# Kernel tuning notes

Measured on AMD Instinct MI355X. Metric: run time of the kernel, lower is better.

Reference implementation:

```python
import jax, jax.numpy as jnp
import numpy as np

NUM_EMB = 1024
DIM = 256
BETA = 0.25


def setup_inputs() -> dict:
    key = jax.random.key(0)
    kx, kc = jax.random.split(key)
    x = jax.random.normal(kx, (32, DIM, 32, 32), dtype=jnp.float32)
    # nn.Parameter(...).uniform_(-1/num_emb, 1/num_emb)
    code_book = jax.random.uniform(kc, (NUM_EMB, DIM), dtype=jnp.float32,
                                   minval=-1.0 / NUM_EMB, maxval=1.0 / NUM_EMB)
    return {"x": x, "code_book": code_book}


def reference(x, code_book):
    b, c, h, w = x.shape
    # (b h w) c
    x_ = x.transpose(0, 2, 3, 1).reshape(-1, c)
    sq = jnp.sum(code_book ** 2, axis=-1)[None, :] + jnp.sum(x_ ** 2, axis=-1)[:, None]
    dist = sq - 2.0 * jnp.einsum('nc,kc->nk', x_, code_book)
    ids = jnp.argmin(dist, axis=-1).reshape(b, h, w)
    emb = code_book[ids]            # [b, h, w, c]
    emb = emb.transpose(0, 3, 1, 2)  # [b, c, h, w]
    dict_loss = jnp.mean((jax.lax.stop_gradient(x) - emb) ** 2)
    commitment_loss = BETA * jnp.mean((x - jax.lax.stop_gradient(emb)) ** 2)
    emb_loss = dict_loss + commitment_loss
    # straight-through estimator
    emb_st = x + jax.lax.stop_gradient(emb - x)
    return ids, emb_st, emb_loss
```

## Files before the change

kernel.cpp:

```cpp
#include <hip/hip_runtime.h>

#define NUM_EMB 1024
#define DIM     256
#define NPIX    32768
#define NELEM   8388608

typedef unsigned short u16;
typedef unsigned int   u32;
typedef __attribute__((ext_vector_type(8))) _Float16 f16x8;
typedef __attribute__((ext_vector_type(4))) float f32x4;

__device__ __forceinline__ u16 f32_f16(float f) {
    _Float16 h = (_Float16)f;
    return __builtin_bit_cast(u16, h);
}
__device__ __forceinline__ float f16_f32(u16 b) {
    return (float)__builtin_bit_cast(_Float16, b);
}


__global__ __launch_bounds__(256) void k_prep_x(const float* __restrict__ x,
        u16* __restrict__ Xa, u16* __restrict__ Xb,
        float* __restrict__ nx_out)
{
    __shared__ float nxp[4][64];
    const int t  = threadIdx.x;
    const int p  = t & 63;
    const int cq = t >> 6;
    const int bi = blockIdx.x;
    const int b  = bi >> 4;
    const int hw = ((bi & 15) << 6) + p;
    const float* xp = x + (((size_t)(b * 256 + cq * 64)) << 10) + hw;
    float s = 0.f;
    for (int i0 = 0; i0 < 64; i0 += 8) {
        u32 qa[4], qb[4];
#pragma unroll
        for (int j = 0; j < 8; ++j) {
            float v = xp[(size_t)(i0 + j) << 10];
            s = fmaf(v, v, s);
            float va = v * 0.25f;
            u16 ha = f32_f16(va);
            float rb = (va - f16_f32(ha)) * 1024.0f;
            u16 hb = f32_f16(rb);
            if ((j & 1) == 0) { qa[j>>1] = ha; qb[j>>1] = hb; }
            else { qa[j>>1] |= (u32)ha << 16; qb[j>>1] |= (u32)hb << 16; }
        }
        const int c = cq * 64 + i0;
        const size_t chunk = (((size_t)((c >> 5) * 4 + ((c >> 3) & 3))) << 15)
                             + (size_t)bi * 64 + p;
        *(uint4*)(Xa + chunk * 8) = make_uint4(qa[0], qa[1], qa[2], qa[3]);
        *(uint4*)(Xb + chunk * 8) = make_uint4(qb[0], qb[1], qb[2], qb[3]);
    }
    nxp[cq][p] = s;
    __syncthreads();
    if (t < 64)
        nx_out[bi * 64 + t] = ((nxp[0][t] + nxp[1][t]) + nxp[2][t]) + nxp[3][t];
}

__global__ __launch_bounds__(256) void k_prep_e(const float* __restrict__ cb,
        u16* __restrict__ Ea, u16* __restrict__ Eb,
        float* __restrict__ ne_out)
{
    const int t = threadIdx.x;
    const int l32 = t & 31;
    const int code = blockIdx.x * 8 + (t >> 5);
    const float* cp = cb + (size_t)code * 256 + l32 * 8;
    u32 qa[4], qb[4];
    float s = 0.f;
#pragma unroll
    for (int j = 0; j < 8; ++j) {
        float v = cp[j];
        s = fmaf(v, v, s);
        float va = v * 2048.0f;
        u16 ha = f32_f16(va);
        float rb = (va - f16_f32(ha)) * 1024.0f;
        u16 hb = f32_f16(rb);
        if ((j & 1) == 0) { qa[j>>1] = ha; qb[j>>1] = hb; }
        else { qa[j>>1] |= (u32)ha << 16; qb[j>>1] |= (u32)hb << 16; }
    }
    const size_t chunk = ((size_t)l32 << 10) + code;
    *(uint4*)(Ea + chunk * 8) = make_uint4(qa[0], qa[1], qa[2], qa[3]);
    *(uint4*)(Eb + chunk * 8) = make_uint4(qb[0], qb[1], qb[2], qb[3]);
#pragma unroll
    for (int off = 16; off > 0; off >>= 1) s += __shfl_xor(s, off);
    if (l32 == 0) ne_out[code] = s;
}

__global__ __launch_bounds__(256, 4) void k_mfma_argmin(
        const u16* __restrict__ XA, const u16* __restrict__ XB,
        const u16* __restrict__ EA, const u16* __restrict__ EB,
        const float* __restrict__ nx, const float* __restrict__ ne,
        float* __restrict__ partV, int* __restrict__ partI)
{
    __shared__ __align__(16) unsigned char ldsA[2][8192];
    __shared__ float redV[4][64];
    __shared__ int   redI[4][64];

    const int t = threadIdx.x;
    const int l = t & 63;
    const int w = t >> 6;

    const int bi   = blockIdx.x;
    const int xcd  = bi & 7;
    const int slot = bi >> 3;
    const int cT   = slot & 7;
    const int pT   = ((slot >> 3) << 3) | xcd;
    const int px0  = pT << 6;
    const int c0   = cT << 7;
    const int n0   = w << 5;
    const int kbl  = l >> 4;
    const int il   = l & 15;

    const u16* Xt[2] = {XA, XB};

    auto stageA = [&](int kc, int bf) {
#pragma unroll
        for (int q = 0; q < 2; ++q) {
            const int kb = t >> 6, px = t & 63;
            const u16* sa = Xt[q] + ((((size_t)(kc * 4 + kb)) << 15) + px0 + px) * 8;
            __builtin_amdgcn_global_load_lds(
                (const __attribute__((address_space(1))) void*)sa,
                (__attribute__((address_space(3))) void*)(&ldsA[bf][q * 4096 + t * 16]),
                16, 0, 0);
        }
    };

    f32x4 acc1[4][2], acc2[4][2];
#pragma unroll
    for (int i = 0; i < 4; ++i)
#pragma unroll
        for (int j = 0; j < 2; ++j) {
            acc1[i][j] = (f32x4){0.f, 0.f, 0.f, 0.f};
            acc2[i][j] = (f32x4){0.f, 0.f, 0.f, 0.f};
        }

    const size_t boff = (size_t)kbl * 8192 + (size_t)(c0 + n0 + il) * 8;
    const u16* pBa = EA + boff;
    const u16* pBb = EB + boff;

    f16x8 bqa[2], bqb[2];
#pragma unroll
    for (int ni = 0; ni < 2; ++ni) {
        bqa[ni] = *(const f16x8*)(pBa + ni * 128);
        bqb[ni] = *(const f16x8*)(pBb + ni * 128);
    }
    stageA(0, 0);
    __syncthreads();

#pragma unroll
    for (int kc = 0; kc < 8; ++kc) {
        const int bf = kc & 1;
        if (kc < 7) stageA(kc + 1, bf ^ 1);

        f16x8 nqa[2], nqb[2];
        if (kc < 7) {
#pragma unroll
            for (int ni = 0; ni < 2; ++ni) {
                nqa[ni] = *(const f16x8*)(pBa + (size_t)(kc + 1) * 32768 + ni * 128);
                nqb[ni] = *(const f16x8*)(pBb + (size_t)(kc + 1) * 32768 + ni * 128);
            }
        }

        __builtin_amdgcn_s_setprio(1);
#pragma unroll
        for (int mi = 0; mi < 4; ++mi) {
            const int fo = (kbl * 64 + mi * 16 + il) * 16;
            f16x8 afa = *(const f16x8*)(&ldsA[bf][fo]);
            f16x8 afb = *(const f16x8*)(&ldsA[bf][4096 + fo]);
#pragma unroll
            for (int ni = 0; ni < 2; ++ni) {
                acc1[mi][ni] = __builtin_amdgcn_mfma_f32_16x16x32_f16(
                    afa, bqa[ni], acc1[mi][ni], 0, 0, 0);
                acc2[mi][ni] = __builtin_amdgcn_mfma_f32_16x16x32_f16(
                    afb, bqa[ni], acc2[mi][ni], 0, 0, 0);
                acc2[mi][ni] = __builtin_amdgcn_mfma_f32_16x16x32_f16(
                    afa, bqb[ni], acc2[mi][ni], 0, 0, 0);
            }
        }
        __builtin_amdgcn_s_setprio(0);

        if (kc < 7) {
            __syncthreads();
#pragma unroll
            for (int ni = 0; ni < 2; ++ni) { bqa[ni] = nqa[ni]; bqb[ni] = nqb[ni]; }
        }
    }

    const int g = kbl, col = il;
    float nev[2];
#pragma unroll
    for (int ni = 0; ni < 2; ++ni) nev[ni] = ne[c0 + n0 + ni * 16 + col];
#pragma unroll
    for (int mi = 0; mi < 4; ++mi) {
#pragma unroll
        for (int r = 0; r < 4; ++r) {
            const int pxl = mi * 16 + g * 4 + r;
            const float nxv = nx[px0 + pxl];
            float best = 3.4e38f; int besti = 0;
#pragma unroll
            for (int ni = 0; ni < 2; ++ni) {
                float tt = fmaf(acc2[mi][ni][r], 9.765625e-04f, acc1[mi][ni][r]);
                float sc = (nxv + nev[ni]) - tt * 3.90625e-03f;
                if (sc < best) { best = sc; besti = c0 + n0 + ni * 16 + col; }
            }
#pragma unroll
            for (int off = 1; off < 16; off <<= 1) {
                float ov = __shfl_xor(best, off);
                int   oi = __shfl_xor(besti, off);
                if (ov < best || (ov == best && oi < besti)) { best = ov; besti = oi; }
            }
            if (col == 0) { redV[w][pxl] = best; redI[w][pxl] = besti; }
        }
    }
    __syncthreads();
    if (t < 64) {
        float bv = redV[0][t]; int bidx = redI[0][t];
#pragma unroll
        for (int q = 1; q < 4; ++q) {
            float v = redV[q][t];
            int   i = redI[q][t];
            if (v < bv || (v == bv && i < bidx)) { bv = v; bidx = i; }
        }
        partV[cT * NPIX + px0 + t] = bv;
        partI[cT * NPIX + px0 + t] = bidx;
    }
}

__global__ __launch_bounds__(256) void k_outputs2(const float* __restrict__ x,
        const float* __restrict__ cb,
        const float* __restrict__ partV, const int* __restrict__ partI,
        float* __restrict__ ids_f, float* __restrict__ out_emb,
        float* __restrict__ partials)
{
    __shared__ int   ids_s[64];
    __shared__ float ev[64][65];
    __shared__ float sm[256];

    const int t  = threadIdx.x;
    const int w  = t >> 6, l = t & 63;
    const int bi = blockIdx.x;
    const int b  = bi >> 4;
    const int hw0 = (bi & 15) << 6;
    const int n0 = (b << 10) + hw0;

    if (t < 64) {
        const int px = n0 + t;
        float bv = partV[px]; int bix = partI[px];
#pragma unroll
        for (int ct = 1; ct < 8; ++ct) {
            float v = partV[ct * NPIX + px];
            int   i = partI[ct * NPIX + px];
            if (v < bv || (v == bv && i < bix)) { bv = v; bix = i; }
        }
        ids_f[px] = (float)bix;
        ids_s[t] = bix;
    }
    __syncthreads();

    float s = 0.f;
    for (int cc = 0; cc < 4; ++cc) {
#pragma unroll
        for (int pp = 0; pp < 16; ++pp) {
            const int px = w * 16 + pp;
            ev[px][l] = cb[(size_t)ids_s[px] * DIM + cc * 64 + l];
        }
        __syncthreads();
#pragma unroll
        for (int ci = 0; ci < 16; ++ci) {
            const int c  = cc * 64 + w * 16 + ci;
            const size_t xi = (((size_t)(b * DIM + c)) << 10) + hw0 + l;
            float xv = x[xi];
            float e  = ev[l][c & 63];
            out_emb[xi] = xv + (e - xv);
            float d = xv - e;
            s = fmaf(d, d, s);
        }
        __syncthreads();
    }
    sm[t] = s;
    __syncthreads();
    for (int off = 128; off > 0; off >>= 1) {
        if (t < off) sm[t] += sm[t + off];
        __syncthreads();
    }
    if (t == 0) partials[bi] = sm[0];
}

__global__ __launch_bounds__(256) void k_finalize(const float* __restrict__ partials,
                                                  int nparts,
                                                  float* __restrict__ out_loss)
{
    __shared__ float sm[256];
    const int tid = threadIdx.x;
    float s = 0.f;
    for (int k = tid; k < nparts; k += 256) s += partials[k];
    sm[tid] = s;
    __syncthreads();
    for (int off = 128; off > 0; off >>= 1) {
        if (tid < off) sm[tid] += sm[tid + off];
        __syncthreads();
    }
    if (tid == 0) {
        float m = sm[0] / (float)NELEM;
        out_loss[0] = m + 0.25f * m;
    }
}

__global__ __launch_bounds__(256) void k_enorm(const float* __restrict__ cb,
                                               float* __restrict__ enorm)
{
    const int tid  = threadIdx.x;
    const int lane = tid & 63;
    const int w    = tid >> 6;
    const int k    = blockIdx.x * 4 + w;
    const float* cp = cb + (size_t)k * DIM;
    float s = 0.f;
#pragma unroll
    for (int t = 0; t < 4; ++t) {
        float v = cp[lane + t * 64];
        s = fmaf(v, v, s);
    }
#pragma unroll
    for (int off = 32; off > 0; off >>= 1) s += __shfl_down(s, off);
    if (lane == 0) enorm[k] = s;
}

__global__ __launch_bounds__(256) void k_argmin(const float* __restrict__ x,
                                                const float* __restrict__ cb,
                                                const float* __restrict__ enorm,
                                                float* __restrict__ out_ids)
{
    __shared__ float xs[32][64];
    __shared__ float cbs[32][68];
    __shared__ float nx_l[64];
    __shared__ float nxp[4][64];
    __shared__ float red_v[64][17];
    __shared__ int   red_i[64][17];

    const int tid  = threadIdx.x;
    const int tx   = tid & 15;
    const int ty   = tid >> 4;
    const int pix0 = blockIdx.x * 64;
    const int b    = pix0 >> 10;
    const int hw0  = pix0 & 1023;

    {
        const int p = tid & 63, q = tid >> 6;
        float s = 0.f;
        const float* xp = x + ((size_t)(b * DIM + q * 64) * 1024) + hw0 + p;
        for (int c = 0; c < 64; ++c) {
            float v = xp[c * 1024];
            s = fmaf(v, v, s);
        }
        nxp[q][p] = s;
        __syncthreads();
        if (tid < 64)
            nx_l[tid] = ((nxp[0][tid] + nxp[1][tid]) + nxp[2][tid]) + nxp[3][tid];
        __syncthreads();
    }

    float nx_r[4];
#pragma unroll
    for (int i = 0; i < 4; ++i) nx_r[i] = nx_l[ty * 4 + i];

    float best_v[4];
    int   best_i[4];
#pragma unroll
    for (int i = 0; i < 4; ++i) { best_v[i] = 3.4e38f; best_i[i] = 0; }

    for (int cc = 0; cc < 16; ++cc) {
        float acc[4][4];
#pragma unroll
        for (int i = 0; i < 4; ++i)
#pragma unroll
            for (int j = 0; j < 4; ++j) acc[i][j] = 0.f;

        for (int kcc = 0; kcc < 8; ++kcc) {
            __syncthreads();
            {
                const int p = tid & 63, k0 = tid >> 6;
                const float* xp = x + ((size_t)(b * DIM + kcc * 32) * 1024) + hw0 + p;
#pragma unroll
                for (int tt = 0; tt < 8; ++tt) {
                    int kk = k0 + tt * 4;
                    xs[kk][p] = xp[kk * 1024];
                }
            }
            {
                const int kk = tid & 31, r0 = tid >> 5;
                const float* cp = cb + (size_t)(cc * 64) * DIM + kcc * 32 + kk;
#pragma unroll
                for (int tt = 0; tt < 8; ++tt) {
                    int r = r0 + tt * 8;
                    cbs[kk][r] = cp[r * DIM];
                }
            }
            __syncthreads();
#pragma unroll
            for (int kk = 0; kk < 32; ++kk) {
                float4 A = *(const float4*)&xs[kk][ty * 4];
                float4 B = *(const float4*)&cbs[kk][tx * 4];
                float a[4] = {A.x, A.y, A.z, A.w};
                float bb[4] = {B.x, B.y, B.z, B.w};
#pragma unroll
                for (int i = 0; i < 4; ++i)
#pragma unroll
                    for (int j = 0; j < 4; ++j)
                        acc[i][j] = fmaf(a[i], bb[j], acc[i][j]);
            }
        }

#pragma unroll
        for (int j = 0; j < 4; ++j) {
            const int code = cc * 64 + tx * 4 + j;
            const float nee = enorm[code];
#pragma unroll
            for (int i = 0; i < 4; ++i) {
                float s = (nx_r[i] + nee) - 2.0f * acc[i][j];
                if (s < best_v[i]) { best_v[i] = s; best_i[i] = code; }
            }
        }
    }

#pragma unroll
    for (int i = 0; i < 4; ++i) {
        red_v[ty * 4 + i][tx] = best_v[i];
        red_i[ty * 4 + i][tx] = best_i[i];
    }
    __syncthreads();
    if (tid < 64) {
        float bv = red_v[tid][0];
        int   bi = red_i[tid][0];
#pragma unroll
        for (int tt = 1; tt < 16; ++tt) {
            float v = red_v[tid][tt];
            int   idx = red_i[tid][tt];
            if (v < bv || (v == bv && idx < bi)) { bv = v; bi = idx; }
        }
        out_ids[pix0 + tid] = (float)bi;
    }
}

__global__ __launch_bounds__(256) void k_outputs(const float* __restrict__ x,
                                                 const float* __restrict__ cb,
                                                 const float* __restrict__ ids_f,
                                                 float* __restrict__ out_emb,
                                                 float* __restrict__ partials)
{
    const int tid = threadIdx.x;
    const int gid = blockIdx.x * 256 + tid;
    float s = 0.f;
#pragma unroll
    for (int it = 0; it < 4; ++it) {
        const int grp = gid + it * 524288;
        const int e0  = grp << 2;
        const int c   = (e0 >> 10) & 255;
        const int b   = e0 >> 18;
        const int hw  = e0 & 1023;
        const int n0  = (b << 10) + hw;
        float4 idv = *(const float4*)(ids_f + n0);
        float4 xv  = *(const float4*)(x + e0);
        float ev0 = cb[(int)idv.x * DIM + c];
        float ev1 = cb[(int)idv.y * DIM + c];
        float ev2 = cb[(int)idv.z * DIM + c];
        float ev3 = cb[(int)idv.w * DIM + c];
        float4 ov;
        ov.x = xv.x + (ev0 - xv.x);
        ov.y = xv.y + (ev1 - xv.y);
        ov.z = xv.z + (ev2 - xv.z);
        ov.w = xv.w + (ev3 - xv.w);
        *(float4*)(out_emb + e0) = ov;
        float d0 = xv.x - ev0, d1 = xv.y - ev1, d2 = xv.z - ev2, d3 = xv.w - ev3;
        s = fmaf(d0, d0, s); s = fmaf(d1, d1, s);
        s = fmaf(d2, d2, s); s = fmaf(d3, d3, s);
    }
    __shared__ float sm[256];
    sm[tid] = s;
    __syncthreads();
    for (int off = 128; off > 0; off >>= 1) {
        if (tid < off) sm[tid] += sm[tid + off];
        __syncthreads();
    }
    if (tid == 0) partials[blockIdx.x] = sm[0];
}

extern "C" void kernel_launch(void* const* d_in, const int* in_sizes, int n_in,
                              void* d_out, int out_size, void* d_ws, size_t ws_size,
                              hipStream_t stream)
{
    const float* x  = (const float*)d_in[0];
    const float* cb = (const float*)d_in[1];
    float* out   = (float*)d_out;
    float* ids_f = out;
    float* emb   = out + NPIX;
    float* loss  = out + NPIX + NELEM;

    char* wsb = (char*)d_ws;
    const size_t NEED = 36843520ull;
    if (ws_size >= NEED) {
        u16*   Xa = (u16*)(wsb);
        u16*   Xb = (u16*)(wsb + 16777216);
        u16*   Ea = (u16*)(wsb + 33554432);
        u16*   Eb = (u16*)(wsb + 34078720);
        float* nx = (float*)(wsb + 34603008);
        float* ne = (float*)(wsb + 34734080);
        float* pV = (float*)(wsb + 34738176);
        int*   pI = (int*)  (wsb + 35786752);
        float* lp = (float*)(wsb + 36835328);
        k_prep_x    <<<512,  256, 0, stream>>>(x, Xa, Xb, nx);
        k_prep_e    <<<128,  256, 0, stream>>>(cb, Ea, Eb, ne);
        k_mfma_argmin<<<4096, 256, 0, stream>>>(Xa, Xb, Ea, Eb, nx, ne, pV, pI);
        k_outputs2  <<<512,  256, 0, stream>>>(x, cb, pV, pI, ids_f, emb, lp);
        k_finalize  <<<1,    256, 0, stream>>>(lp, 512, loss);
    } else {
        float* partials = (float*)wsb;
        float* enorm    = partials + 2048;
        k_enorm   <<<256,  256, 0, stream>>>(cb, enorm);
        k_argmin  <<<512,  256, 0, stream>>>(x, cb, enorm, ids_f);
        k_outputs <<<2048, 256, 0, stream>>>(x, cb, ids_f, emb, partials);
        k_finalize<<<1,    256, 0, stream>>>(partials, 2048, loss);
    }
}
```

Baseline: 105.9 us.

## Deepen A-tile LDS pipeline to four buffers with prefetch distance two

Grows the shared A staging buffer from two to four slots and issues async global-to-LDS loads two k-chunks ahead. The per-iteration __syncthreads is replaced by explicit vmcnt waits plus raw s_barrier inside sched_barriers, so only the oldest stage has to land. B fragments are now loaded at the top of each iteration rather than prefetched one chunk ahead. The aim is to hide global latency better, at the cost of double the LDS (which may lower occupancy at 4 blocks/CU) and hand-counted vmcnt values that could be wrong, because the B loads also count toward vmcnt.

```diff
diff --git a/kernel.cpp b/kernel.cpp
--- a/kernel.cpp
+++ b/kernel.cpp
@@ -92,7 +92,7 @@
         const float* __restrict__ nx, const float* __restrict__ ne,
         float* __restrict__ partV, int* __restrict__ partI)
 {
-    __shared__ __align__(16) unsigned char ldsA[2][8192];
+    __shared__ __align__(16) unsigned char ldsA[4][8192];
     __shared__ float redV[4][64];
     __shared__ int   redI[4][64];
 
@@ -138,28 +138,24 @@
     const u16* pBa = EA + boff;
     const u16* pBb = EB + boff;
 
-    f16x8 bqa[2], bqb[2];
-#pragma unroll
-    for (int ni = 0; ni < 2; ++ni) {
-        bqa[ni] = *(const f16x8*)(pBa + ni * 128);
-        bqb[ni] = *(const f16x8*)(pBb + ni * 128);
-    }
     stageA(0, 0);
-    __syncthreads();
+    stageA(1, 1);
+    __builtin_amdgcn_sched_barrier(0);
+    asm volatile("s_waitcnt vmcnt(2)" ::: "memory");
+    __builtin_amdgcn_s_barrier();
+    __builtin_amdgcn_sched_barrier(0);
 
 #pragma unroll
     for (int kc = 0; kc < 8; ++kc) {
-        const int bf = kc & 1;
-        if (kc < 7) stageA(kc + 1, bf ^ 1);
-
-        f16x8 nqa[2], nqb[2];
-        if (kc < 7) {
-#pragma unroll
-            for (int ni = 0; ni < 2; ++ni) {
-                nqa[ni] = *(const f16x8*)(pBa + (size_t)(kc + 1) * 32768 + ni * 128);
-                nqb[ni] = *(const f16x8*)(pBb + (size_t)(kc + 1) * 32768 + ni * 128);
-            }
-        }
+        const int bf = kc & 3;
+
+        f16x8 bqa[2], bqb[2];
+#pragma unroll
+        for (int ni = 0; ni < 2; ++ni) {
+            bqa[ni] = *(const f16x8*)(pBa + (size_t)kc * 32768 + ni * 128);
+            bqb[ni] = *(const f16x8*)(pBb + (size_t)kc * 32768 + ni * 128);
+        }
+        if (kc < 6) stageA(kc + 2, (kc + 2) & 3);
 
         __builtin_amdgcn_s_setprio(1);
 #pragma unroll
@@ -180,9 +176,13 @@
         __builtin_amdgcn_s_setprio(0);
 
         if (kc < 7) {
-            __syncthreads();
-#pragma unroll
-            for (int ni = 0; ni < 2; ++ni) { bqa[ni] = nqa[ni]; bqb[ni] = nqb[ni]; }
+            __builtin_amdgcn_sched_barrier(0);
+            if (kc < 6)
+                asm volatile("s_waitcnt vmcnt(2)" ::: "memory");
+            else
+                asm volatile("s_waitcnt vmcnt(0)" ::: "memory");
+            __builtin_amdgcn_s_barrier();
+            __builtin_amdgcn_sched_barrier(0);
         }
     }
 
```

After: 105.5 us, median of 2. Within noise of the previous version (-0.4%).
